# Kernel optimization log

Hardware: AMD Instinct MI355X
Metric: run time of the kernel (lower is better)

The kernel has to match this reference:

```python
import jax, jax.numpy as jnp
import numpy as np

N = 50000       # nodes
E = 600000      # edges
F_IN = 500      # num_feature
H = 64          # hidden_dim (ODE state = 2*H)
C = 40          # num_class
T = 1.0         # integration time
STEPS = 4       # RK4 steps (16 ODE function evals)


def setup_inputs() -> dict:
    key = jax.random.key(0)
    ks = jax.random.split(key, 7)
    x = jax.random.normal(ks[0], (N, F_IN), dtype=jnp.float32)
    edge_src = jax.random.randint(ks[1], (E,), 0, N, dtype=jnp.int32)
    edge_dst = jax.random.randint(ks[2], (E,), 0, N, dtype=jnp.int32)
    edge_w = jax.random.uniform(ks[3], (E,), dtype=jnp.float32)
    m1_w = jax.random.normal(ks[4], (F_IN, H), dtype=jnp.float32) / np.sqrt(F_IN).astype(np.float32)
    m1_b = jnp.zeros((H,), jnp.float32)
    alpha_train = jnp.ones((N,), jnp.float32)  # alpha * ones(N) with alpha=1.0
    m2_w = jax.random.normal(ks[5], (H, C), dtype=jnp.float32) / np.sqrt(H).astype(np.float32)
    m2_b = jnp.zeros((C,), jnp.float32)
    return dict(x=x, edge_w=edge_w, m1_w=m1_w, m1_b=m1_b,
                alpha_train=alpha_train, m2_w=m2_w, m2_b=m2_b,
                edge_src=edge_src, edge_dst=edge_dst)


def spmm(edge_src, edge_dst, edge_w, z):
    # A @ z where A[i,j] = sum of edge_w over edges (src=i, dst=j)
    msg = edge_w[:, None] * z[edge_dst]           # [E, 2H]
    return jax.ops.segment_sum(msg, edge_src, num_segments=N)


def reference(x, edge_w, m1_w, m1_b, alpha_train, m2_w, m2_b, edge_src, edge_dst):
    # Encoder (dropout is identity in eval mode)
    h = x @ m1_w + m1_b                           # [N, H]
    h = jnp.concatenate([h, jnp.zeros_like(h)], axis=1)  # [N, 2H]
    x0 = jax.lax.stop_gradient(h)                 # x0 = x.clone().detach()
    alph = jax.nn.sigmoid(alpha_train)[:, None]   # [N, 1]

    def f(z):  # ODE RHS: sigmoid(alpha)*0.5*(A z - z) + x0
        az = spmm(edge_src, edge_dst, edge_w, z)
        return alph * 0.5 * (az - z) + x0

    dt = jnp.float32(T / STEPS)

    def step(z, _):
        k1 = f(z)
        k2 = f(z + 0.5 * dt * k1)
        k3 = f(z + 0.5 * dt * k2)
        k4 = f(z + dt * k3)
        return z + (dt / 6.0) * (k1 + 2.0 * k2 + 2.0 * k3 + k4), None

    z, _ = jax.lax.scan(step, h, None, length=STEPS)
    z = jax.nn.relu(z[:, :H])                     # first half of state
    return z @ m2_w + m2_b                        # [N, C]
```

## Files before the change

### kernel.cpp

```cpp
#include <hip/hip_runtime.h>
#include <hip/hip_fp16.h>

#define N_NODES 50000
#define N_EDGES 600000
#define F_IN    500
#define H_DIM   64
#define C_OUT   40
#define STEPS   4
#define NB_SCAN ((N_NODES + 255) / 256)
#define KTILES  16
#define XS_COLS 516

using half8 = __attribute__((ext_vector_type(8))) _Float16;
using f32x4 = __attribute__((ext_vector_type(4))) float;

__global__ __launch_bounds__(256) void bfrag_kernel(
    const float* __restrict__ W, __half* __restrict__ bfrag)
{
    int t = blockIdx.x * 256 + threadIdx.x;
    if (t >= KTILES * 4 * 64) return;
    int lane = t & 63;
    int c    = (t >> 6) & 3;
    int kt   = t >> 8;
    int col  = c * 16 + (lane & 15);
    int kb   = kt * 32 + (lane >> 4) * 8;
    union { uint4 u; __half h[8]; } v;
    #pragma unroll
    for (int j = 0; j < 8; ++j) {
        int k = kb + j;
        v.h[j] = (k < F_IN) ? __float2half(W[(size_t)k * H_DIM + col]) : __half(0.f);
    }
    *reinterpret_cast<uint4*>(bfrag + (size_t)t * 8) = v.u;
}

__global__ __launch_bounds__(256) void encoder_kernel(
    const float* __restrict__ x, const __half* __restrict__ bfrag,
    const float* __restrict__ b, __half* __restrict__ x0H,
    __half* __restrict__ zH)
{
    __shared__ __align__(16) float xs[16][XS_COLS];
    __shared__ f32x4 red[3][64][4];
    __shared__ float outs[16][68];

    int t    = threadIdx.x;
    int wave = t >> 6;
    int lane = t & 63;
    int r0   = blockIdx.x * 16;

    #pragma unroll
    for (int i = 0; i < 8; ++i) {
        int c = i * 64 + lane;
        if (c < 500) {
            int row = c / 125;
            int cc  = c - row * 125;
            int grow = r0 + wave * 4 + row;
            if (grow >= N_NODES) grow = N_NODES - 1;
            float4 v = *reinterpret_cast<const float4*>(x + (size_t)grow * F_IN + cc * 4);
            *reinterpret_cast<float4*>(&xs[wave * 4 + row][cc * 4]) = v;
        }
    }
    xs[t >> 4][500 + (t & 15)] = 0.f;
    __syncthreads();

    int rowl = lane & 15;
    int kg   = lane >> 4;
    const uint4* bf = reinterpret_cast<const uint4*>(bfrag);

    f32x4 acc[4];
    #pragma unroll
    for (int c = 0; c < 4; ++c) acc[c] = (f32x4){0.f, 0.f, 0.f, 0.f};

    int ktb = wave * 4;
    #pragma unroll
    for (int ki = 0; ki < 4; ++ki) {
        int kt = ktb + ki;
        int k0 = kt * 32 + kg * 8;
        float4 xa = *reinterpret_cast<const float4*>(&xs[rowl][k0]);
        float4 xb = *reinterpret_cast<const float4*>(&xs[rowl][k0 + 4]);
        half8 a;
        a[0] = (_Float16)xa.x; a[1] = (_Float16)xa.y;
        a[2] = (_Float16)xa.z; a[3] = (_Float16)xa.w;
        a[4] = (_Float16)xb.x; a[5] = (_Float16)xb.y;
        a[6] = (_Float16)xb.z; a[7] = (_Float16)xb.w;
        #pragma unroll
        for (int c = 0; c < 4; ++c) {
            union { uint4 u; half8 h; } bv;
            bv.u = bf[(size_t)(kt * 4 + c) * 64 + lane];
            acc[c] = __builtin_amdgcn_mfma_f32_16x16x32_f16(a, bv.h, acc[c], 0, 0, 0);
        }
    }

    if (wave > 0) {
        #pragma unroll
        for (int c = 0; c < 4; ++c) red[wave - 1][lane][c] = acc[c];
    }
    __syncthreads();
    if (wave == 0) {
        #pragma unroll
        for (int w = 0; w < 3; ++w)
            #pragma unroll
            for (int c = 0; c < 4; ++c) {
                f32x4 r = red[w][lane][c];
                acc[c][0] += r[0]; acc[c][1] += r[1];
                acc[c][2] += r[2]; acc[c][3] += r[3];
            }
        #pragma unroll
        for (int c = 0; c < 4; ++c) {
            int col = c * 16 + rowl;
            float bias = b[col];
            #pragma unroll
            for (int r = 0; r < 4; ++r)
                outs[kg * 4 + r][col] = acc[c][r] + bias;
        }
        int orow = lane >> 2;
        int ocb  = (lane & 3) * 16;
        int grow = r0 + orow;
        if (grow < N_NODES) {
            union { uint4 u[2]; __half h[16]; } pk;
            #pragma unroll
            for (int i = 0; i < 16; ++i) pk.h[i] = __float2half(outs[orow][ocb + i]);
            size_t idx = (size_t)grow * H_DIM + ocb;
            *reinterpret_cast<uint4*>(zH  + idx)     = pk.u[0];
            *reinterpret_cast<uint4*>(zH  + idx + 8) = pk.u[1];
            *reinterpret_cast<uint4*>(x0H + idx)     = pk.u[0];
            *reinterpret_cast<uint4*>(x0H + idx + 8) = pk.u[1];
        }
    }
}

__global__ void hist_kernel(const int* __restrict__ src, int* __restrict__ counts)
{
    int e = blockIdx.x * 256 + threadIdx.x;
    if (e < N_EDGES) atomicAdd(&counts[src[e]], 1);
}

__global__ __launch_bounds__(256) void scanA_kernel(
    const int* __restrict__ counts, int* __restrict__ blockSums)
{
    __shared__ int red[256];
    int i = blockIdx.x * 256 + threadIdx.x;
    red[threadIdx.x] = (i < N_NODES) ? counts[i] : 0;
    __syncthreads();
    #pragma unroll
    for (int s = 128; s > 0; s >>= 1) {
        if (threadIdx.x < s) red[threadIdx.x] += red[threadIdx.x + s];
        __syncthreads();
    }
    if (threadIdx.x == 0) blockSums[blockIdx.x] = red[0];
}

__global__ __launch_bounds__(256) void scanB_kernel(
    const int* __restrict__ blockSums, int* __restrict__ blockBases)
{
    __shared__ int s[256];
    int tid = threadIdx.x;
    int v = (tid < NB_SCAN) ? blockSums[tid] : 0;
    s[tid] = v;
    __syncthreads();
    #pragma unroll
    for (int d = 1; d < 256; d <<= 1) {
        int t = (tid >= d) ? s[tid - d] : 0;
        __syncthreads();
        s[tid] += t;
        __syncthreads();
    }
    if (tid < NB_SCAN) blockBases[tid] = s[tid] - v;
}

__global__ __launch_bounds__(256) void scanC_kernel(
    const int* __restrict__ counts, const int* __restrict__ blockBases,
    int* __restrict__ off, int* __restrict__ cursor)
{
    __shared__ int s[256];
    int tid = threadIdx.x;
    int i = blockIdx.x * 256 + tid;
    int v = (i < N_NODES) ? counts[i] : 0;
    s[tid] = v;
    __syncthreads();
    #pragma unroll
    for (int d = 1; d < 256; d <<= 1) {
        int t = (tid >= d) ? s[tid - d] : 0;
        __syncthreads();
        s[tid] += t;
        __syncthreads();
    }
    if (i < N_NODES) {
        int excl = blockBases[blockIdx.x] + s[tid] - v;
        off[i] = excl;
        cursor[i] = excl;
        if (i == N_NODES - 1) off[N_NODES] = excl + v;
    }
}

__global__ void scatter_kernel(const int* __restrict__ src, const int* __restrict__ dst,
                               const float* __restrict__ w,
                               int* __restrict__ cursor, unsigned* __restrict__ epack)
{
    int e = blockIdx.x * 256 + threadIdx.x;
    if (e < N_EDGES) {
        int s = src[e];
        int p = atomicAdd(&cursor[s], 1);
        unsigned wh = (unsigned)__half_as_ushort(__float2half(w[e]));
        epack[p] = (unsigned)dst[e] | (wh << 16);
    }
}

template<int STAGE>
__global__ __launch_bounds__(256) void stage_kernel(
    const int* __restrict__ off, const unsigned* __restrict__ epack,
    const __half* __restrict__ zsH, const __half* __restrict__ zH,
    const __half* __restrict__ x0H, const float* __restrict__ alpha,
    __half* __restrict__ accH, __half* __restrict__ outH, float cnext)
{
    int node = blockIdx.x * 32 + (threadIdx.x >> 3);
    if (node >= N_NODES) return;
    int cb = (threadIdx.x & 7) << 4;
    int c  = cb >> 1;

    int jb = off[node], je = off[node + 1];
    const char* rdB = reinterpret_cast<const char*>(zsH);

    union H4 { uint4 u; __half2 h[4]; };
    union HW { unsigned short us; __half h; };

    float azA[8], azB[8];
    #pragma unroll
    for (int i = 0; i < 8; ++i) { azA[i] = 0.f; azB[i] = 0.f; }

#define WOF(E)  ((size_t)((E) & 0xFFFFu) << 7)
#define WGT(E)  ({ HW hw_; hw_.us = (unsigned short)((E) >> 16); __half2float(hw_.h); })
#define ACC8(dst, V, W)                                                    \
    {                                                                      \
        float2 f0 = __half22float2((V).h[0]);                              \
        float2 f1 = __half22float2((V).h[1]);                              \
        float2 f2 = __half22float2((V).h[2]);                              \
        float2 f3 = __half22float2((V).h[3]);                              \
        dst[0] = fmaf(W, f0.x, dst[0]); dst[1] = fmaf(W, f0.y, dst[1]);    \
        dst[2] = fmaf(W, f1.x, dst[2]); dst[3] = fmaf(W, f1.y, dst[3]);    \
        dst[4] = fmaf(W, f2.x, dst[4]); dst[5] = fmaf(W, f2.y, dst[5]);    \
        dst[6] = fmaf(W, f3.x, dst[6]); dst[7] = fmaf(W, f3.y, dst[7]);    \
    }

    int j = jb;
    for (; j + 3 < je; j += 4) {
        unsigned e0 = epack[j];
        unsigned e1 = epack[j + 1];
        unsigned e2 = epack[j + 2];
        unsigned e3 = epack[j + 3];
        H4 v0, v1, v2, v3;
        v0.u = *reinterpret_cast<const uint4*>(rdB + WOF(e0) + cb);
        v1.u = *reinterpret_cast<const uint4*>(rdB + WOF(e1) + cb);
        v2.u = *reinterpret_cast<const uint4*>(rdB + WOF(e2) + cb);
        v3.u = *reinterpret_cast<const uint4*>(rdB + WOF(e3) + cb);
        float w0 = WGT(e0), w1 = WGT(e1), w2 = WGT(e2), w3 = WGT(e3);
        ACC8(azA, v0, w0);
        ACC8(azB, v1, w1);
        ACC8(azA, v2, w2);
        ACC8(azB, v3, w3);
    }
    for (; j < je; ++j) {
        unsigned e0 = epack[j];
        H4 v0;
        v0.u = *reinterpret_cast<const uint4*>(rdB + WOF(e0) + cb);
        float w0 = WGT(e0);
        ACC8(azA, v0, w0);
    }
#undef ACC8
#undef WOF
#undef WGT

    float az[8];
    #pragma unroll
    for (int i = 0; i < 8; ++i) az[i] = azA[i] + azB[i];

    size_t idx = (size_t)node * H_DIM + c;
    H4 sr; sr.u = *reinterpret_cast<const uint4*>(zsH + idx);
    float s[8];
    {
        float2 f0 = __half22float2(sr.h[0]), f1 = __half22float2(sr.h[1]);
        float2 f2 = __half22float2(sr.h[2]), f3 = __half22float2(sr.h[3]);
        s[0] = f0.x; s[1] = f0.y; s[2] = f1.x; s[3] = f1.y;
        s[4] = f2.x; s[5] = f2.y; s[6] = f3.x; s[7] = f3.y;
    }
    H4 xr; xr.u = *reinterpret_cast<const uint4*>(x0H + idx);
    float xv[8];
    {
        float2 f0 = __half22float2(xr.h[0]), f1 = __half22float2(xr.h[1]);
        float2 f2 = __half22float2(xr.h[2]), f3 = __half22float2(xr.h[3]);
        xv[0] = f0.x; xv[1] = f0.y; xv[2] = f1.x; xv[3] = f1.y;
        xv[4] = f2.x; xv[5] = f2.y; xv[6] = f3.x; xv[7] = f3.y;
    }
    float a = 0.5f / (1.f + __expf(-alpha[node]));

    float k[8];
    #pragma unroll
    for (int i = 0; i < 8; ++i) k[i] = fmaf(a, az[i] - s[i], xv[i]);

    float o[8];
    if constexpr (STAGE == 0) {
        H4 aw;
        aw.h[0] = __float22half2_rn(make_float2(k[0], k[1]));
        aw.h[1] = __float22half2_rn(make_float2(k[2], k[3]));
        aw.h[2] = __float22half2_rn(make_float2(k[4], k[5]));
        aw.h[3] = __float22half2_rn(make_float2(k[6], k[7]));
        *reinterpret_cast<uint4*>(accH + idx) = aw.u;
        #pragma unroll
        for (int i = 0; i < 8; ++i) o[i] = fmaf(cnext, k[i], s[i]);
    } else if constexpr (STAGE == 1 || STAGE == 2) {
        H4 ar; ar.u = *reinterpret_cast<const uint4*>(accH + idx);
        float av[8];
        {
            float2 f0 = __half22float2(ar.h[0]), f1 = __half22float2(ar.h[1]);
            float2 f2 = __half22float2(ar.h[2]), f3 = __half22float2(ar.h[3]);
            av[0] = f0.x; av[1] = f0.y; av[2] = f1.x; av[3] = f1.y;
            av[4] = f2.x; av[5] = f2.y; av[6] = f3.x; av[7] = f3.y;
        }
        #pragma unroll
        for (int i = 0; i < 8; ++i) av[i] = fmaf(2.f, k[i], av[i]);
        H4 aw;
        aw.h[0] = __float22half2_rn(make_float2(av[0], av[1]));
        aw.h[1] = __float22half2_rn(make_float2(av[2], av[3]));
        aw.h[2] = __float22half2_rn(make_float2(av[4], av[5]));
        aw.h[3] = __float22half2_rn(make_float2(av[6], av[7]));
        *reinterpret_cast<uint4*>(accH + idx) = aw.u;
        H4 br; br.u = *reinterpret_cast<const uint4*>(zH + idx);
        float bv[8];
        {
            float2 f0 = __half22float2(br.h[0]), f1 = __half22float2(br.h[1]);
            float2 f2 = __half22float2(br.h[2]), f3 = __half22float2(br.h[3]);
            bv[0] = f0.x; bv[1] = f0.y; bv[2] = f1.x; bv[3] = f1.y;
            bv[4] = f2.x; bv[5] = f2.y; bv[6] = f3.x; bv[7] = f3.y;
        }
        #pragma unroll
        for (int i = 0; i < 8; ++i) o[i] = fmaf(cnext, k[i], bv[i]);
    } else {
        H4 ar; ar.u = *reinterpret_cast<const uint4*>(accH + idx);
        float av[8];
        {
            float2 f0 = __half22float2(ar.h[0]), f1 = __half22float2(ar.h[1]);
            float2 f2 = __half22float2(ar.h[2]), f3 = __half22float2(ar.h[3]);
            av[0] = f0.x; av[1] = f0.y; av[2] = f1.x; av[3] = f1.y;
            av[4] = f2.x; av[5] = f2.y; av[6] = f3.x; av[7] = f3.y;
        }
        H4 br; br.u = *reinterpret_cast<const uint4*>(zH + idx);
        float bv[8];
        {
            float2 f0 = __half22float2(br.h[0]), f1 = __half22float2(br.h[1]);
            float2 f2 = __half22float2(br.h[2]), f3 = __half22float2(br.h[3]);
            bv[0] = f0.x; bv[1] = f0.y; bv[2] = f1.x; bv[3] = f1.y;
            bv[4] = f2.x; bv[5] = f2.y; bv[6] = f3.x; bv[7] = f3.y;
        }
        #pragma unroll
        for (int i = 0; i < 8; ++i) o[i] = fmaf(cnext, av[i] + k[i], bv[i]);
    }
    H4 sv;
    sv.h[0] = __float22half2_rn(make_float2(o[0], o[1]));
    sv.h[1] = __float22half2_rn(make_float2(o[2], o[3]));
    sv.h[2] = __float22half2_rn(make_float2(o[4], o[5]));
    sv.h[3] = __float22half2_rn(make_float2(o[6], o[7]));
    *reinterpret_cast<uint4*>(outH + idx) = sv.u;
}

__global__ __launch_bounds__(256) void decoder_kernel(
    const __half* __restrict__ zH, const float* __restrict__ W2,
    const float* __restrict__ b2, float* __restrict__ out)
{
    __shared__ float zsm[4][H_DIM];
    int lane = threadIdx.x & 63;
    int w    = threadIdx.x >> 6;
    int node = blockIdx.x * 4 + w;
    int ld   = node >= N_NODES ? N_NODES - 1 : node;
    float zv = __half2float(zH[(size_t)ld * H_DIM + lane]);
    zsm[w][lane] = zv > 0.f ? zv : 0.f;
    __syncthreads();
    if (node < N_NODES && lane < C_OUT) {
        float acc = b2[lane];
        #pragma unroll
        for (int k = 0; k < H_DIM; ++k)
            acc = fmaf(zsm[w][k], W2[k * C_OUT + lane], acc);
        out[(size_t)node * C_OUT + lane] = acc;
    }
}

extern "C" void kernel_launch(void* const* d_in, const int* in_sizes, int n_in,
                              void* d_out, int out_size, void* d_ws, size_t ws_size,
                              hipStream_t stream)
{
    const float* x     = (const float*)d_in[0];
    const float* ew    = (const float*)d_in[1];
    const float* m1w   = (const float*)d_in[2];
    const float* m1b   = (const float*)d_in[3];
    const float* alpha = (const float*)d_in[4];
    const float* m2w   = (const float*)d_in[5];
    const float* m2b   = (const float*)d_in[6];
    const int*   esrc  = (const int*)d_in[7];
    const int*   edst  = (const int*)d_in[8];
    float* out = (float*)d_out;

    char* ws = (char*)d_ws;
    size_t o = 0;
    auto alloc = [&](size_t bytes) -> void* {
        void* p = ws + o;
        o = (o + bytes + 255) & ~(size_t)255;
        return p;
    };
    __half*   x0H    = (__half*)alloc((size_t)N_NODES * H_DIM * 2);
    __half*   zH     = (__half*)alloc((size_t)N_NODES * H_DIM * 2);
    __half*   ztAH   = (__half*)alloc((size_t)N_NODES * H_DIM * 2);
    __half*   ztBH   = (__half*)alloc((size_t)N_NODES * H_DIM * 2);
    __half*   accH   = (__half*)alloc((size_t)N_NODES * H_DIM * 2);
    __half*   bfrag  = (__half*)alloc((size_t)KTILES * 4 * 64 * 8 * 2);
    int*      counts = (int*)alloc((size_t)N_NODES * 4);
    int*      off    = (int*)alloc((size_t)(N_NODES + 1) * 4);
    int*      cursor = (int*)alloc((size_t)N_NODES * 4);
    int*      bsums  = (int*)alloc((size_t)NB_SCAN * 4);
    int*      bbases = (int*)alloc((size_t)NB_SCAN * 4);
    unsigned* epack  = (unsigned*)alloc((size_t)N_EDGES * 4);

    hipMemsetAsync(counts, 0, (size_t)N_NODES * 4, stream);
    hist_kernel<<<(N_EDGES + 255) / 256, 256, 0, stream>>>(esrc, counts);
    scanA_kernel<<<NB_SCAN, 256, 0, stream>>>(counts, bsums);
    scanB_kernel<<<1, 256, 0, stream>>>(bsums, bbases);
    scanC_kernel<<<NB_SCAN, 256, 0, stream>>>(counts, bbases, off, cursor);
    scatter_kernel<<<(N_EDGES + 255) / 256, 256, 0, stream>>>(esrc, edst, ew, cursor, epack);

    bfrag_kernel<<<(KTILES * 4 * 64 + 255) / 256, 256, 0, stream>>>(m1w, bfrag);
    encoder_kernel<<<(N_NODES + 15) / 16, 256, 0, stream>>>(x, bfrag, m1b, x0H, zH);

    const float dt = 1.0f / STEPS;
    int sgrid = (N_NODES + 31) / 32;
    for (int step = 0; step < STEPS; ++step) {
        stage_kernel<0><<<sgrid, 256, 0, stream>>>(off, epack, zH,   zH, x0H, alpha, accH, ztAH, 0.5f * dt);
        stage_kernel<1><<<sgrid, 256, 0, stream>>>(off, epack, ztAH, zH, x0H, alpha, accH, ztBH, 0.5f * dt);
        stage_kernel<2><<<sgrid, 256, 0, stream>>>(off, epack, ztBH, zH, x0H, alpha, accH, ztAH, dt);
        stage_kernel<3><<<sgrid, 256, 0, stream>>>(off, epack, ztAH, zH, x0H, alpha, accH, zH,   dt / 6.0f);
    }

    decoder_kernel<<<(N_NODES + 3) / 4, 256, 0, stream>>>(zH, m2w, m2b, out);
}
```

Measured before the change: 363.4 us.

## Drop RK4 accumulator buffer by reconstructing k-sum from stage states

Removes the accH accumulator that each RK4 stage read and rewrote. The final stage instead rebuilds the weighted k sum from the stored intermediate states ztA, ztB and ztC using the identity k_i = (zt_i - z)/c. The per-node loads are now issued before the neighbour gather, and the gather loop is unrolled to 8 edges to keep more loads in flight. This cuts several read/write passes over the state per step. In exchange it needs one extra state buffer, adds three reads in the last stage, and accumulates fp16 rounding error differently.

```diff
diff --git a/kernel.cpp b/kernel.cpp
--- a/kernel.cpp
+++ b/kernel.cpp
@@ -210,18 +210,30 @@
     const int* __restrict__ off, const unsigned* __restrict__ epack,
     const __half* __restrict__ zsH, const __half* __restrict__ zH,
     const __half* __restrict__ x0H, const float* __restrict__ alpha,
-    __half* __restrict__ accH, __half* __restrict__ outH, float cnext)
+    const __half* __restrict__ ztA, const __half* __restrict__ ztB,
+    __half* __restrict__ outH, float cnext)
 {
     int node = blockIdx.x * 32 + (threadIdx.x >> 3);
     if (node >= N_NODES) return;
     int cb = (threadIdx.x & 7) << 4;
     int c  = cb >> 1;
 
+    size_t idx = (size_t)node * H_DIM + c;
+    union H4 { uint4 u; __half2 h[4]; };
+    union HW { unsigned short us; __half h; };
+
+    H4 sr; sr.u = *reinterpret_cast<const uint4*>(zsH + idx);
+    H4 xr; xr.u = *reinterpret_cast<const uint4*>(x0H + idx);
+    H4 br, ar, b2r;
+    if constexpr (STAGE != 0) br.u = *reinterpret_cast<const uint4*>(zH + idx);
+    if constexpr (STAGE == 3) {
+        ar.u  = *reinterpret_cast<const uint4*>(ztA + idx);
+        b2r.u = *reinterpret_cast<const uint4*>(ztB + idx);
+    }
+    float alr = alpha[node];
+
     int jb = off[node], je = off[node + 1];
     const char* rdB = reinterpret_cast<const char*>(zsH);
-
-    union H4 { uint4 u; __half2 h[4]; };
-    union HW { unsigned short us; __half h; };
 
     float azA[8], azB[8];
     #pragma unroll
@@ -242,28 +254,41 @@
     }
 
     int j = jb;
+    for (; j + 7 < je; j += 8) {
+        unsigned e0 = epack[j],     e1 = epack[j + 1];
+        unsigned e2 = epack[j + 2], e3 = epack[j + 3];
+        unsigned e4 = epack[j + 4], e5 = epack[j + 5];
+        unsigned e6 = epack[j + 6], e7 = epack[j + 7];
+        H4 v0, v1, v2, v3, v4, v5, v6, v7;
+        v0.u = *reinterpret_cast<const uint4*>(rdB + WOF(e0) + cb);
+        v1.u = *reinterpret_cast<const uint4*>(rdB + WOF(e1) + cb);
+        v2.u = *reinterpret_cast<const uint4*>(rdB + WOF(e2) + cb);
+        v3.u = *reinterpret_cast<const uint4*>(rdB + WOF(e3) + cb);
+        v4.u = *reinterpret_cast<const uint4*>(rdB + WOF(e4) + cb);
+        v5.u = *reinterpret_cast<const uint4*>(rdB + WOF(e5) + cb);
+        v6.u = *reinterpret_cast<const uint4*>(rdB + WOF(e6) + cb);
+        v7.u = *reinterpret_cast<const uint4*>(rdB + WOF(e7) + cb);
+        ACC8(azA, v0, WGT(e0)); ACC8(azB, v1, WGT(e1));
+        ACC8(azA, v2, WGT(e2)); ACC8(azB, v3, WGT(e3));
+        ACC8(azA, v4, WGT(e4)); ACC8(azB, v5, WGT(e5));
+        ACC8(azA, v6, WGT(e6)); ACC8(azB, v7, WGT(e7));
+    }
     for (; j + 3 < je; j += 4) {
-        unsigned e0 = epack[j];
-        unsigned e1 = epack[j + 1];
-        unsigned e2 = epack[j + 2];
-        unsigned e3 = epack[j + 3];
+        unsigned e0 = epack[j],     e1 = epack[j + 1];
+        unsigned e2 = epack[j + 2], e3 = epack[j + 3];
         H4 v0, v1, v2, v3;
         v0.u = *reinterpret_cast<const uint4*>(rdB + WOF(e0) + cb);
         v1.u = *reinterpret_cast<const uint4*>(rdB + WOF(e1) + cb);
         v2.u = *reinterpret_cast<const uint4*>(rdB + WOF(e2) + cb);
         v3.u = *reinterpret_cast<const uint4*>(rdB + WOF(e3) + cb);
-        float w0 = WGT(e0), w1 = WGT(e1), w2 = WGT(e2), w3 = WGT(e3);
-        ACC8(azA, v0, w0);
-        ACC8(azB, v1, w1);
-        ACC8(azA, v2, w2);
-        ACC8(azB, v3, w3);
+        ACC8(azA, v0, WGT(e0)); ACC8(azB, v1, WGT(e1));
+        ACC8(azA, v2, WGT(e2)); ACC8(azB, v3, WGT(e3));
     }
     for (; j < je; ++j) {
         unsigned e0 = epack[j];
         H4 v0;
         v0.u = *reinterpret_cast<const uint4*>(rdB + WOF(e0) + cb);
-        float w0 = WGT(e0);
-        ACC8(azA, v0, w0);
+        ACC8(azA, v0, WGT(e0));
     }
 #undef ACC8
 #undef WOF
@@ -273,8 +298,6 @@
     #pragma unroll
     for (int i = 0; i < 8; ++i) az[i] = azA[i] + azB[i];
 
-    size_t idx = (size_t)node * H_DIM + c;
-    H4 sr; sr.u = *reinterpret_cast<const uint4*>(zsH + idx);
     float s[8];
     {
         float2 f0 = __half22float2(sr.h[0]), f1 = __half22float2(sr.h[1]);
@@ -282,7 +305,6 @@
         s[0] = f0.x; s[1] = f0.y; s[2] = f1.x; s[3] = f1.y;
         s[4] = f2.x; s[5] = f2.y; s[6] = f3.x; s[7] = f3.y;
     }
-    H4 xr; xr.u = *reinterpret_cast<const uint4*>(x0H + idx);
     float xv[8];
     {
         float2 f0 = __half22float2(xr.h[0]), f1 = __half22float2(xr.h[1]);
@@ -290,7 +312,7 @@
         xv[0] = f0.x; xv[1] = f0.y; xv[2] = f1.x; xv[3] = f1.y;
         xv[4] = f2.x; xv[5] = f2.y; xv[6] = f3.x; xv[7] = f3.y;
     }
-    float a = 0.5f / (1.f + __expf(-alpha[node]));
+    float a = 0.5f / (1.f + __expf(-alr));
 
     float k[8];
     #pragma unroll
@@ -298,32 +320,9 @@
 
     float o[8];
     if constexpr (STAGE == 0) {
-        H4 aw;
-        aw.h[0] = __float22half2_rn(make_float2(k[0], k[1]));
-        aw.h[1] = __float22half2_rn(make_float2(k[2], k[3]));
-        aw.h[2] = __float22half2_rn(make_float2(k[4], k[5]));
-        aw.h[3] = __float22half2_rn(make_float2(k[6], k[7]));
-        *reinterpret_cast<uint4*>(accH + idx) = aw.u;
         #pragma unroll
         for (int i = 0; i < 8; ++i) o[i] = fmaf(cnext, k[i], s[i]);
     } else if constexpr (STAGE == 1 || STAGE == 2) {
-        H4 ar; ar.u = *reinterpret_cast<const uint4*>(accH + idx);
-        float av[8];
-        {
-            float2 f0 = __half22float2(ar.h[0]), f1 = __half22float2(ar.h[1]);
-            float2 f2 = __half22float2(ar.h[2]), f3 = __half22float2(ar.h[3]);
-            av[0] = f0.x; av[1] = f0.y; av[2] = f1.x; av[3] = f1.y;
-            av[4] = f2.x; av[5] = f2.y; av[6] = f3.x; av[7] = f3.y;
-        }
-        #pragma unroll
-        for (int i = 0; i < 8; ++i) av[i] = fmaf(2.f, k[i], av[i]);
-        H4 aw;
-        aw.h[0] = __float22half2_rn(make_float2(av[0], av[1]));
-        aw.h[1] = __float22half2_rn(make_float2(av[2], av[3]));
-        aw.h[2] = __float22half2_rn(make_float2(av[4], av[5]));
-        aw.h[3] = __float22half2_rn(make_float2(av[6], av[7]));
-        *reinterpret_cast<uint4*>(accH + idx) = aw.u;
-        H4 br; br.u = *reinterpret_cast<const uint4*>(zH + idx);
         float bv[8];
         {
             float2 f0 = __half22float2(br.h[0]), f1 = __half22float2(br.h[1]);
@@ -334,24 +333,31 @@
         #pragma unroll
         for (int i = 0; i < 8; ++i) o[i] = fmaf(cnext, k[i], bv[i]);
     } else {
-        H4 ar; ar.u = *reinterpret_cast<const uint4*>(accH + idx);
-        float av[8];
+        float bv[8], av[8], b2v[8];
+        {
+            float2 f0 = __half22float2(br.h[0]), f1 = __half22float2(br.h[1]);
+            float2 f2 = __half22float2(br.h[2]), f3 = __half22float2(br.h[3]);
+            bv[0] = f0.x; bv[1] = f0.y; bv[2] = f1.x; bv[3] = f1.y;
+            bv[4] = f2.x; bv[5] = f2.y; bv[6] = f3.x; bv[7] = f3.y;
+        }
         {
             float2 f0 = __half22float2(ar.h[0]), f1 = __half22float2(ar.h[1]);
             float2 f2 = __half22float2(ar.h[2]), f3 = __half22float2(ar.h[3]);
             av[0] = f0.x; av[1] = f0.y; av[2] = f1.x; av[3] = f1.y;
             av[4] = f2.x; av[5] = f2.y; av[6] = f3.x; av[7] = f3.y;
         }
-        H4 br; br.u = *reinterpret_cast<const uint4*>(zH + idx);
-        float bv[8];
         {
-            float2 f0 = __half22float2(br.h[0]), f1 = __half22float2(br.h[1]);
-            float2 f2 = __half22float2(br.h[2]), f3 = __half22float2(br.h[3]);
-            bv[0] = f0.x; bv[1] = f0.y; bv[2] = f1.x; bv[3] = f1.y;
-            bv[4] = f2.x; bv[5] = f2.y; bv[6] = f3.x; bv[7] = f3.y;
-        }
-        #pragma unroll
-        for (int i = 0; i < 8; ++i) o[i] = fmaf(cnext, av[i] + k[i], bv[i]);
+            float2 f0 = __half22float2(b2r.h[0]), f1 = __half22float2(b2r.h[1]);
+            float2 f2 = __half22float2(b2r.h[2]), f3 = __half22float2(b2r.h[3]);
+            b2v[0] = f0.x; b2v[1] = f0.y; b2v[2] = f1.x; b2v[3] = f1.y;
+            b2v[4] = f2.x; b2v[5] = f2.y; b2v[6] = f3.x; b2v[7] = f3.y;
+        }
+        const float c13 = 1.f / 3.f, c23 = 2.f / 3.f;
+        #pragma unroll
+        for (int i = 0; i < 8; ++i) {
+            float d = c13 * (av[i] - bv[i]) + c23 * (b2v[i] - bv[i]) + c13 * (s[i] - bv[i]);
+            o[i] = bv[i] + d + cnext * k[i];
+        }
     }
     H4 sv;
     sv.h[0] = __float22half2_rn(make_float2(o[0], o[1]));
@@ -408,7 +414,7 @@
     __half*   zH     = (__half*)alloc((size_t)N_NODES * H_DIM * 2);
     __half*   ztAH   = (__half*)alloc((size_t)N_NODES * H_DIM * 2);
     __half*   ztBH   = (__half*)alloc((size_t)N_NODES * H_DIM * 2);
-    __half*   accH   = (__half*)alloc((size_t)N_NODES * H_DIM * 2);
+    __half*   ztCH   = (__half*)alloc((size_t)N_NODES * H_DIM * 2);
     __half*   bfrag  = (__half*)alloc((size_t)KTILES * 4 * 64 * 8 * 2);
     int*      counts = (int*)alloc((size_t)N_NODES * 4);
     int*      off    = (int*)alloc((size_t)(N_NODES + 1) * 4);
@@ -430,10 +436,10 @@
     const float dt = 1.0f / STEPS;
     int sgrid = (N_NODES + 31) / 32;
     for (int step = 0; step < STEPS; ++step) {
-        stage_kernel<0><<<sgrid, 256, 0, stream>>>(off, epack, zH,   zH, x0H, alpha, accH, ztAH, 0.5f * dt);
-        stage_kernel<1><<<sgrid, 256, 0, stream>>>(off, epack, ztAH, zH, x0H, alpha, accH, ztBH, 0.5f * dt);
-        stage_kernel<2><<<sgrid, 256, 0, stream>>>(off, epack, ztBH, zH, x0H, alpha, accH, ztAH, dt);
-        stage_kernel<3><<<sgrid, 256, 0, stream>>>(off, epack, ztAH, zH, x0H, alpha, accH, zH,   dt / 6.0f);
+        stage_kernel<0><<<sgrid, 256, 0, stream>>>(off, epack, zH,   zH, x0H, alpha, nullptr, nullptr, ztAH, 0.5f * dt);
+        stage_kernel<1><<<sgrid, 256, 0, stream>>>(off, epack, ztAH, zH, x0H, alpha, nullptr, nullptr, ztBH, 0.5f * dt);
+        stage_kernel<2><<<sgrid, 256, 0, stream>>>(off, epack, ztBH, zH, x0H, alpha, nullptr, nullptr, ztCH, dt);
+        stage_kernel<3><<<sgrid, 256, 0, stream>>>(off, epack, ztCH, zH, x0H, alpha, ztAH,   ztBH,    zH,   dt / 6.0f);
     }
 
     decoder_kernel<<<(N_NODES + 3) / 4, 256, 0, stream>>>(zH, m2w, m2b, out);
```

Measured after the change: 403.2 us. +10.9%, slower.
